# Kernel optimization log

Hardware: AMD Instinct MI355X
Metric: run time of the kernel (lower is better)

The kernel has to match this reference:

```python
import jax, jax.numpy as jnp
import numpy as np

# Problem sizes (see shape_source)
C = 4096                      # sparse matrix is C x C
NUMEL = C * C                 # 16,777,216
S = 3355443                   # round(NUMEL * 0.2) sampled gradient entries
R = 1048576                   # result_quantity (top-k buffer size)
DECAY = 0.95                  # decay_constant
FRAC = S / float(NUMEL)       # fractional_sparsity (mask_active=False branch)


def setup_inputs() -> dict:
    key = jax.random.key(0)
    k1, k2, k3, k4 = jax.random.split(key, 4)
    # Sampled linear indices into the C x C grid (forward: torch.randint(0, numel, [S]))
    sample_index = jax.random.randint(k1, (S,), 0, NUMEL, dtype=jnp.int32)
    # Steady-state buffer of (row, col) pairs and their running gradient magnitudes
    result_index = jax.random.randint(k2, (R, 2), 0, C, dtype=jnp.int32)
    result_value = jax.random.uniform(k3, (R,), dtype=jnp.float32)
    # Incoming gradient on the sampled accumulator entries
    gradient = jax.random.normal(k4, (S,), dtype=jnp.float32)
    return {
        "sample_index": sample_index,
        "result_index": result_index,
        "result_value": result_value,
        "gradient": gradient,
    }


def reference(sample_index, result_index, result_value, gradient):
    """Faithful JAX version of StochasticSubSampler's backward-hook update:
    decay the stored buffer, take |gradient| on the new samples, coalesce
    duplicated (row, col) entries by summation, then keep the top-R values.
    Returns (new_result_index [R,2] int32, new_result_value [R] float32)."""
    adj_decay = 1.0 - FRAC * (1.0 - DECAY)  # adjusted decay constant

    # Linearized keys for coalescing. sample_index is already row*C + col.
    samp_keys = sample_index
    res_keys = result_index[:, 0] * C + result_index[:, 1]
    keys = jnp.concatenate([samp_keys, res_keys])               # [K]
    vals = jnp.concatenate([jnp.abs(gradient), adj_decay * result_value])  # [K]
    K = keys.shape[0]

    # Coalesce: sum values that share the same (row, col) key.
    uniq, inv = jnp.unique(keys, size=K, fill_value=-1, return_inverse=True)
    summed = jax.ops.segment_sum(vals, inv, num_segments=K)     # [K]
    counts = jax.ops.segment_sum(jnp.ones_like(vals), inv, num_segments=K)
    neg = jnp.finfo(jnp.float32).min
    summed = jnp.where(counts > 0, summed, neg)  # mask padded unique slots

    # Descending sort + top-R selection (argsort(-v)[:R] in the original).
    top_vals, top_pos = jax.lax.top_k(summed, R)
    top_keys = uniq[top_pos]
    new_index = jnp.stack([top_keys // C, top_keys % C], axis=-1)  # [R, 2]
    return new_index, top_vals
```

## Files before the change

kernel.cpp:

```cpp
#include <hip/hip_runtime.h>
#include <stdint.h>

#define CDIM   4096
#define S_N    3355443
#define R_N    1048576
#define N1     (S_N + R_N)
#define TILE   4096
#define WPT    (TILE / 256)
#define NTILES ((N1 + TILE - 1) / TILE)
#define NPAD   (NTILES * TILE)
#define NSB    (NPAD / 256)
#define SR_CH  ((NTILES + 255) / 256)
#define PAD_KEY 0xFFFFFFu
#define PAD_VAL 0xFFFFFFFFu
#define SENT  (((uint64_t)PAD_KEY << 32) | (uint64_t)PAD_VAL)

static __device__ __forceinline__ unsigned blockScanExcl(unsigned v, unsigned t,
                                                         unsigned* lw, unsigned* tot){
  unsigned lane = t & 63u, w = t >> 6;
  unsigned x = v;
  #pragma unroll
  for (int off = 1; off < 64; off <<= 1){
    unsigned y = __shfl_up(x, off, 64);
    if (lane >= (unsigned)off) x += y;
  }
  if (lane == 63u) lw[w] = x;
  __syncthreads();
  unsigned woff = 0;
  for (unsigned i = 0; i < w; i++) woff += lw[i];
  *tot = lw[0] + lw[1] + lw[2] + lw[3];
  __syncthreads();
  return x + woff - v;
}

__global__ __launch_bounds__(256) void k_build(const int* __restrict__ sidx,
                                               const int* __restrict__ ridx,
                                               const float* __restrict__ rval,
                                               const float* __restrict__ grad,
                                               uint64_t* __restrict__ A,
                                               unsigned* __restrict__ gh){
  __shared__ unsigned h[256];
  unsigned t = threadIdx.x;
  h[t] = 0; __syncthreads();
  size_t base = (size_t)blockIdx.x * TILE;
  #pragma unroll
  for (int r = 0; r < WPT; r++){
    unsigned i = (unsigned)(base + (size_t)r*256 + t);
    uint32_t key, vb;
    if (i < S_N){
      key = (uint32_t)sidx[i];
      vb  = __float_as_uint(fabsf(grad[i]));
    } else if (i < N1){
      unsigned j = i - S_N;
      int2 rc = ((const int2* __restrict__)ridx)[j];
      key = (uint32_t)(rc.x * CDIM + rc.y);
      const float ADJF = (float)(1.0 - (3355443.0 / 16777216.0) * (1.0 - 0.95));
      vb = __float_as_uint(ADJF * rval[j]);
    } else {
      key = PAD_KEY; vb = PAD_VAL;
    }
    A[i] = ((uint64_t)key << 32) | (uint64_t)vb;
    atomicAdd(&h[key & 0xFFu], 1u);
  }
  __syncthreads();
  gh[t * NTILES + blockIdx.x] = h[t];
}

__global__ __launch_bounds__(256) void k_hist(const uint64_t* __restrict__ in, unsigned shift,
                                              unsigned* __restrict__ gh){
  __shared__ unsigned h[256];
  unsigned t = threadIdx.x;
  h[t] = 0; __syncthreads();
  size_t base = (size_t)blockIdx.x * TILE;
  #pragma unroll
  for (int r = 0; r < WPT; r++){
    uint64_t e = in[base + (size_t)r*256 + t];
    atomicAdd(&h[(unsigned)((e >> shift) & 0xFF)], 1u);
  }
  __syncthreads();
  gh[t * NTILES + blockIdx.x] = h[t];
}

__global__ __launch_bounds__(256) void k_hist_syn(const uint64_t* __restrict__ in, unsigned shift,
                                                  unsigned* __restrict__ gh,
                                                  const unsigned* __restrict__ nsyn){
  __shared__ unsigned h[256];
  unsigned t = threadIdx.x;
  unsigned Un = nsyn[0];
  size_t base = (size_t)blockIdx.x * TILE;
  if (base >= (size_t)Un){
    gh[t * NTILES + blockIdx.x] = (t == 255u) ? (unsigned)TILE : 0u;
    return;
  }
  h[t] = 0; __syncthreads();
  #pragma unroll
  for (int r = 0; r < WPT; r++){
    unsigned i = (unsigned)(base + (size_t)r*256 + t);
    uint64_t e = (i < Un) ? in[i] : SENT;
    atomicAdd(&h[(unsigned)((e >> shift) & 0xFF)], 1u);
  }
  __syncthreads();
  gh[t * NTILES + blockIdx.x] = h[t];
}

__global__ __launch_bounds__(256) void k_scanrows(unsigned* __restrict__ gh,
                                                  unsigned* __restrict__ dtot){
  __shared__ unsigned lw[4];
  unsigned d = blockIdx.x, t = threadIdx.x;
  unsigned rowbase = d * NTILES;
  unsigned vals[SR_CH];
  unsigned s = 0;
  #pragma unroll
  for (int k = 0; k < SR_CH; k++){
    unsigned i = t * SR_CH + (unsigned)k;
    vals[k] = (i < NTILES) ? gh[rowbase + i] : 0u;
    s += vals[k];
  }
  unsigned tot;
  unsigned carry = blockScanExcl(s, t, lw, &tot);
  #pragma unroll
  for (int k = 0; k < SR_CH; k++){
    unsigned i = t * SR_CH + (unsigned)k;
    if (i < NTILES){ gh[rowbase + i] = carry; carry += vals[k]; }
  }
  if (t == 0) dtot[d] = tot;
}

__global__ __launch_bounds__(256) void k_cut(const unsigned* __restrict__ dtot,
                                             unsigned* __restrict__ mvar){
  __shared__ unsigned lw[4];
  unsigned t = threadIdx.x;
  unsigned v = dtot[t];
  unsigned tot;
  unsigned excl = blockScanExcl(v, t, lw, &tot);
  unsigned incl = excl + v;
  if (excl < R_N && incl >= R_N) mvar[0] = incl;
}

template <int MODE>
__device__ __forceinline__ void scatter_body(const uint64_t* __restrict__ in,
                                             uint64_t* __restrict__ out,
                                             float* __restrict__ fout,
                                             unsigned shift,
                                             const unsigned* __restrict__ gh,
                                             const unsigned* __restrict__ dtot,
                                             const unsigned* __restrict__ nsyn,
                                             const unsigned* __restrict__ mskip){
  unsigned Un = 0u, M = 0u;
  if (MODE != 0){
    Un = nsyn[0]; M = mskip[0];
    if ((unsigned)blockIdx.x * TILE >= Un && M <= Un) return;
  }
  __shared__ unsigned wrun[4*256];
  __shared__ unsigned gput[256];
  __shared__ unsigned lw[4];
  __shared__ uint64_t stage[TILE];
  unsigned t = threadIdx.x, lane = t & 63u, w = t >> 6;
  wrun[t] = 0; wrun[256+t] = 0; wrun[512+t] = 0; wrun[768+t] = 0;
  __syncthreads();
  uint64_t ltm = (lane == 0) ? 0ull : (~0ull >> (64u - lane));
  uint64_t elems[WPT]; unsigned rnk[WPT]; unsigned dg[WPT];
  size_t base = (size_t)blockIdx.x * TILE + (size_t)w * (TILE/4);
  #pragma unroll
  for (int r = 0; r < WPT; r++){
    unsigned idx = (unsigned)(base + (size_t)r*64) + lane;
    uint64_t e;
    if (MODE != 0) e = (idx < Un) ? in[idx] : SENT;
    else           e = in[idx];
    elems[r] = e;
    unsigned d = (unsigned)((e >> shift) & 0xFF);
    uint64_t m = ~0ull;
    #pragma unroll
    for (int b = 0; b < 8; b++){
      uint64_t bb = __ballot((d >> b) & 1u);
      m &= ((d >> b) & 1u) ? bb : ~bb;
    }
    unsigned rr   = (unsigned)__popcll(m & ltm);
    unsigned prev = wrun[w*256 + d];
    __builtin_amdgcn_wave_barrier();
    if (rr == 0) wrun[w*256 + d] = prev + (unsigned)__popcll(m);
    __builtin_amdgcn_wave_barrier();
    rnk[r] = prev + rr;
    dg[r]  = d;
  }
  __syncthreads();
  {
    unsigned d = t;
    unsigned c0 = wrun[d], c1 = wrun[256+d], c2 = wrun[512+d], c3 = wrun[768+d];
    unsigned cnt = c0 + c1 + c2 + c3;
    unsigned tot;
    unsigned ldig  = blockScanExcl(cnt, t, lw, &tot);
    unsigned tot2;
    unsigned dbase = blockScanExcl(dtot[d], t, lw, &tot2);
    gput[d] = dbase + gh[d * NTILES + blockIdx.x] - ldig;
    wrun[d]       = ldig;
    wrun[256 + d] = ldig + c0;
    wrun[512 + d] = ldig + c0 + c1;
    wrun[768 + d] = ldig + c0 + c1 + c2;
  }
  __syncthreads();
  #pragma unroll
  for (int r = 0; r < WPT; r++)
    stage[ wrun[w*256 + dg[r]] + rnk[r] ] = elems[r];
  __syncthreads();
  #pragma unroll
  for (int r = 0; r < WPT; r++){
    unsigned j = (unsigned)r * 256u + t;
    uint64_t e = stage[j];
    unsigned d = (unsigned)((e >> shift) & 0xFF);
    unsigned dest = gput[d] + j;
    if (MODE == 2){
      if (dest < R_N){
        uint32_t key = (uint32_t)(e >> 32);
        fout[2u*dest]        = (float)(key >> 12);
        fout[2u*dest + 1u]   = (float)(key & 4095u);
        fout[2u*R_N + dest]  = __uint_as_float(~(uint32_t)e);
      }
    } else if (MODE == 1){
      if (dest < M) out[dest] = e;
    } else {
      out[dest] = e;
    }
  }
}

__global__ __launch_bounds__(256) void k_scatter(const uint64_t* __restrict__ in,
                                                 uint64_t* __restrict__ out,
                                                 unsigned shift,
                                                 const unsigned* __restrict__ gh,
                                                 const unsigned* __restrict__ dtot){
  scatter_body<0>(in, out, nullptr, shift, gh, dtot, nullptr, nullptr);
}

__global__ __launch_bounds__(256) void k_scatter_m(const uint64_t* __restrict__ in,
                                                   uint64_t* __restrict__ out,
                                                   unsigned shift,
                                                   const unsigned* __restrict__ gh,
                                                   const unsigned* __restrict__ dtot,
                                                   const unsigned* __restrict__ nsyn,
                                                   const unsigned* __restrict__ mskip){
  scatter_body<1>(in, out, nullptr, shift, gh, dtot, nsyn, mskip);
}

__global__ __launch_bounds__(256) void k_scatter_out(const uint64_t* __restrict__ in,
                                                     float* __restrict__ fout,
                                                     unsigned shift,
                                                     const unsigned* __restrict__ gh,
                                                     const unsigned* __restrict__ dtot,
                                                     const unsigned* __restrict__ nsyn){
  scatter_body<2>(in, nullptr, fout, shift, gh, dtot, nsyn, nsyn);
}

__global__ __launch_bounds__(256) void k_headcount(const uint64_t* __restrict__ in,
                                                   unsigned* __restrict__ hcnt){
  __shared__ unsigned wc[4];
  unsigned t = threadIdx.x, lane = t & 63u, w = t >> 6;
  size_t p = (size_t)blockIdx.x * 256 + t;
  uint64_t e = in[p];
  uint32_t k = (uint32_t)(e >> 32);
  bool head = ((p == 0) || ((uint32_t)(in[p-1] >> 32) != k)) && ((uint32_t)e != PAD_VAL);
  uint64_t m = __ballot(head);
  if (lane == 0) wc[w] = (unsigned)__popcll(m);
  __syncthreads();
  if (t == 0) hcnt[blockIdx.x] = wc[0] + wc[1] + wc[2] + wc[3];
}

__global__ __launch_bounds__(256) void k_scanheads(unsigned* __restrict__ hcnt,
                                                   unsigned* __restrict__ utot){
  __shared__ unsigned short buf[NSB];
  __shared__ unsigned lw[4];
  unsigned t = threadIdx.x;
  for (unsigned i = t; i < NSB; i += 256) buf[i] = (unsigned short)hcnt[i];
  __syncthreads();
  const unsigned CH = (NSB + 255) / 256;
  unsigned s = 0;
  for (unsigned k = 0; k < CH; k++){
    unsigned i = t * CH + k;
    if (i < NSB) s += buf[i];
  }
  unsigned tot;
  unsigned carry = blockScanExcl(s, t, lw, &tot);
  for (unsigned k = 0; k < CH; k++){
    unsigned i = t * CH + k;
    if (i < NSB){ unsigned v = buf[i]; hcnt[i] = carry; carry += v; }
  }
  if (t == 0) utot[0] = tot;
}

__global__ __launch_bounds__(256) void k_segsum(const uint64_t* __restrict__ in,
                                                uint64_t* __restrict__ out,
                                                const unsigned* __restrict__ hbase){
  __shared__ unsigned wc[4], woffs[4];
  unsigned t = threadIdx.x, lane = t & 63u, w = t >> 6;
  size_t p = (size_t)blockIdx.x * 256 + t;
  uint64_t e0 = in[p];
  uint32_t k = (uint32_t)(e0 >> 32);
  bool head = ((p == 0) || ((uint32_t)(in[p-1] >> 32) != k)) && ((uint32_t)e0 != PAD_VAL);
  uint64_t m = __ballot(head);
  if (lane == 0) wc[w] = (unsigned)__popcll(m);
  __syncthreads();
  if (t == 0){ unsigned a = 0; for (int i = 0; i < 4; i++){ woffs[i] = a; a += wc[i]; } }
  __syncthreads();
  if (head){
    uint64_t ltm = (lane == 0) ? 0ull : (~0ull >> (64u - lane));
    unsigned rank = (unsigned)__popcll(m & ltm);
    unsigned oidx = hbase[blockIdx.x] + woffs[w] + rank;
    float s = __uint_as_float((uint32_t)e0);
    size_t q = p + 1;
    while (q < NPAD){
      uint64_t e = in[q];
      if ((uint32_t)(e >> 32) != k) break;
      uint32_t vb = (uint32_t)e;
      if (vb == PAD_VAL) break;
      s += __uint_as_float(vb);
      q++;
    }
    out[oidx] = ((uint64_t)k << 32) | (uint64_t)(uint32_t)(~__float_as_uint(s));
  }
}

extern "C" void kernel_launch(void* const* d_in, const int* in_sizes, int n_in,
                              void* d_out, int out_size, void* d_ws, size_t ws_size,
                              hipStream_t stream) {
  const int*   sidx = (const int*)d_in[0];
  const int*   ridx = (const int*)d_in[1];
  const float* rval = (const float*)d_in[2];
  const float* grad = (const float*)d_in[3];
  float* out = (float*)d_out;

  uint64_t* A0   = (uint64_t*)d_ws;
  uint64_t* A1   = A0 + NPAD;
  unsigned* gh   = (unsigned*)(A1 + NPAD);
  unsigned* dtot = gh + 256 * NTILES;
  unsigned* hcnt = dtot + 256;
  unsigned* utot = hcnt + NSB;
  unsigned* mvar = utot + 1;

  k_build<<<NTILES, 256, 0, stream>>>(sidx, ridx, rval, grad, A0, gh);

  k_scanrows<<<256,    256, 0, stream>>>(gh, dtot);
  k_scatter <<<NTILES, 256, 0, stream>>>(A0, A1, 32, gh, dtot);
  k_hist    <<<NTILES, 256, 0, stream>>>(A1, 40, gh);
  k_scanrows<<<256,    256, 0, stream>>>(gh, dtot);
  k_scatter <<<NTILES, 256, 0, stream>>>(A1, A0, 40, gh, dtot);
  k_hist    <<<NTILES, 256, 0, stream>>>(A0, 48, gh);
  k_scanrows<<<256,    256, 0, stream>>>(gh, dtot);
  k_scatter <<<NTILES, 256, 0, stream>>>(A0, A1, 48, gh, dtot);

  k_headcount<<<NSB, 256, 0, stream>>>(A1, hcnt);
  k_scanheads<<<1,   256, 0, stream>>>(hcnt, utot);
  k_segsum   <<<NSB, 256, 0, stream>>>(A1, A0, hcnt);

  k_hist_syn <<<NTILES, 256, 0, stream>>>(A0, 24, gh, utot);
  k_scanrows <<<256,    256, 0, stream>>>(gh, dtot);
  k_cut      <<<1,      256, 0, stream>>>(dtot, mvar);
  k_scatter_m<<<NTILES, 256, 0, stream>>>(A0, A1, 24, gh, dtot, utot, mvar);

  k_hist_syn <<<NTILES, 256, 0, stream>>>(A1, 0, gh, mvar);
  k_scanrows <<<256,    256, 0, stream>>>(gh, dtot);
  k_scatter_m<<<NTILES, 256, 0, stream>>>(A1, A0, 0, gh, dtot, mvar, mvar);
  k_hist_syn <<<NTILES, 256, 0, stream>>>(A0, 8, gh, mvar);
  k_scanrows <<<256,    256, 0, stream>>>(gh, dtot);
  k_scatter_m<<<NTILES, 256, 0, stream>>>(A0, A1, 8, gh, dtot, mvar, mvar);
  k_hist_syn <<<NTILES, 256, 0, stream>>>(A1, 16, gh, mvar);
  k_scanrows <<<256,    256, 0, stream>>>(gh, dtot);
  k_scatter_m<<<NTILES, 256, 0, stream>>>(A1, A0, 16, gh, dtot, mvar, mvar);
  k_hist_syn   <<<NTILES, 256, 0, stream>>>(A0, 24, gh, mvar);
  k_scanrows   <<<256,    256, 0, stream>>>(gh, dtot);
  k_scatter_out<<<NTILES, 256, 0, stream>>>(A0, out, 24, gh, dtot, mvar);
}
```

Before: 410.3 us.

## Fuse head-count, scan and segment-sum into single-pass decoupled-lookback coalesce kernel

Replaces the three-kernel coalescing stage (per-block head count, single-block scan, segment sum) with one kernel. It computes per-tile head counts, uses decoupled look-back through a flag/value buffer to get each tile's global output offset, then writes the summed segments. The look-back buffer is zeroed inside the preceding scatter kernel, so no extra memset launch is needed. This saves two launches and one full read of the sorted array, at the cost of inter-block spin-waiting that depends on tiles being scheduled in order.

New measurement: 464.6 us. 1.13x slower.

```diff
diff --git a/kernel.cpp b/kernel.cpp
--- a/kernel.cpp
+++ b/kernel.cpp
@@ -9,7 +9,6 @@
 #define WPT    (TILE / 256)
 #define NTILES ((N1 + TILE - 1) / TILE)
 #define NPAD   (NTILES * TILE)
-#define NSB    (NPAD / 256)
 #define SR_CH  ((NTILES + 255) / 256)
 #define PAD_KEY 0xFFFFFFu
 #define PAD_VAL 0xFFFFFFFFu
@@ -228,7 +227,9 @@
                                                  uint64_t* __restrict__ out,
                                                  unsigned shift,
                                                  const unsigned* __restrict__ gh,
-                                                 const unsigned* __restrict__ dtot){
+                                                 const unsigned* __restrict__ dtot,
+                                                 unsigned* __restrict__ zclr){
+  if (zclr != nullptr && threadIdx.x == 0u) zclr[blockIdx.x] = 0u;
   scatter_body<0>(in, out, nullptr, shift, gh, dtot, nullptr, nullptr);
 }
 
@@ -251,71 +252,101 @@
   scatter_body<2>(in, nullptr, fout, shift, gh, dtot, nsyn, nsyn);
 }
 
-__global__ __launch_bounds__(256) void k_headcount(const uint64_t* __restrict__ in,
-                                                   unsigned* __restrict__ hcnt){
-  __shared__ unsigned wc[4];
-  unsigned t = threadIdx.x, lane = t & 63u, w = t >> 6;
-  size_t p = (size_t)blockIdx.x * 256 + t;
-  uint64_t e = in[p];
-  uint32_t k = (uint32_t)(e >> 32);
-  bool head = ((p == 0) || ((uint32_t)(in[p-1] >> 32) != k)) && ((uint32_t)e != PAD_VAL);
-  uint64_t m = __ballot(head);
-  if (lane == 0) wc[w] = (unsigned)__popcll(m);
-  __syncthreads();
-  if (t == 0) hcnt[blockIdx.x] = wc[0] + wc[1] + wc[2] + wc[3];
-}
-
-__global__ __launch_bounds__(256) void k_scanheads(unsigned* __restrict__ hcnt,
-                                                   unsigned* __restrict__ utot){
-  __shared__ unsigned short buf[NSB];
-  __shared__ unsigned lw[4];
-  unsigned t = threadIdx.x;
-  for (unsigned i = t; i < NSB; i += 256) buf[i] = (unsigned short)hcnt[i];
-  __syncthreads();
-  const unsigned CH = (NSB + 255) / 256;
-  unsigned s = 0;
-  for (unsigned k = 0; k < CH; k++){
-    unsigned i = t * CH + k;
-    if (i < NSB) s += buf[i];
-  }
-  unsigned tot;
-  unsigned carry = blockScanExcl(s, t, lw, &tot);
-  for (unsigned k = 0; k < CH; k++){
-    unsigned i = t * CH + k;
-    if (i < NSB){ unsigned v = buf[i]; hcnt[i] = carry; carry += v; }
-  }
-  if (t == 0) utot[0] = tot;
-}
-
-__global__ __launch_bounds__(256) void k_segsum(const uint64_t* __restrict__ in,
-                                                uint64_t* __restrict__ out,
-                                                const unsigned* __restrict__ hbase){
-  __shared__ unsigned wc[4], woffs[4];
-  unsigned t = threadIdx.x, lane = t & 63u, w = t >> 6;
-  size_t p = (size_t)blockIdx.x * 256 + t;
-  uint64_t e0 = in[p];
-  uint32_t k = (uint32_t)(e0 >> 32);
-  bool head = ((p == 0) || ((uint32_t)(in[p-1] >> 32) != k)) && ((uint32_t)e0 != PAD_VAL);
-  uint64_t m = __ballot(head);
-  if (lane == 0) wc[w] = (unsigned)__popcll(m);
-  __syncthreads();
-  if (t == 0){ unsigned a = 0; for (int i = 0; i < 4; i++){ woffs[i] = a; a += wc[i]; } }
-  __syncthreads();
-  if (head){
-    uint64_t ltm = (lane == 0) ? 0ull : (~0ull >> (64u - lane));
-    unsigned rank = (unsigned)__popcll(m & ltm);
-    unsigned oidx = hbase[blockIdx.x] + woffs[w] + rank;
-    float s = __uint_as_float((uint32_t)e0);
-    size_t q = p + 1;
-    while (q < NPAD){
-      uint64_t e = in[q];
-      if ((uint32_t)(e >> 32) != k) break;
-      uint32_t vb = (uint32_t)e;
-      if (vb == PAD_VAL) break;
-      s += __uint_as_float(vb);
-      q++;
-    }
-    out[oidx] = ((uint64_t)k << 32) | (uint64_t)(uint32_t)(~__float_as_uint(s));
+__global__ __launch_bounds__(256) void k_coalesce(const uint64_t* __restrict__ in,
+                                                  uint64_t* __restrict__ out,
+                                                  unsigned* __restrict__ lb,
+                                                  unsigned* __restrict__ utot){
+  __shared__ unsigned wrc[64];
+  __shared__ unsigned woffs[64];
+  __shared__ unsigned hb;
+  unsigned b = blockIdx.x, t = threadIdx.x, lane = t & 63u, w = t >> 6;
+  size_t base = (size_t)b * TILE;
+  unsigned flags = 0u;
+  #pragma unroll
+  for (int r = 0; r < WPT; r++){
+    size_t p = base + (size_t)r*256 + t;
+    uint64_t e = in[p];
+    uint32_t k = (uint32_t)(e >> 32);
+    uint32_t kp = (uint32_t)__shfl_up((int)k, 1, 64);
+    if (lane == 0u) kp = (p == 0) ? 0u : (uint32_t)(in[p-1] >> 32);
+    bool head = ((p == 0) || (kp != k)) && ((uint32_t)e != PAD_VAL);
+    flags |= (head ? 1u : 0u) << r;
+    unsigned long long m = __ballot(head);
+    if (lane == 0u) wrc[(unsigned)r*4u + w] = (unsigned)__popcll(m);
+  }
+  __syncthreads();
+  if (w == 0u){
+    unsigned v = wrc[lane];
+    unsigned x = v;
+    #pragma unroll
+    for (int off = 1; off < 64; off <<= 1){
+      unsigned y = __shfl_up(x, off, 64);
+      if (lane >= (unsigned)off) x += y;
+    }
+    woffs[lane] = x - v;
+    unsigned cnt = (unsigned)__shfl((int)x, 63);
+    if (lane == 0u)
+      __hip_atomic_store(&lb[b], ((b == 0u) ? (2u<<30) : (1u<<30)) | cnt,
+                         __ATOMIC_RELEASE, __HIP_MEMORY_SCOPE_AGENT);
+    unsigned run = 0u;
+    if (b > 0u){
+      int p0 = (int)b - 1;
+      for (;;){
+        int idx = p0 - (int)lane;
+        unsigned v2 = (idx >= 0)
+          ? __hip_atomic_load(&lb[idx], __ATOMIC_ACQUIRE, __HIP_MEMORY_SCOPE_AGENT)
+          : (2u << 30);
+        if (__ballot((v2 >> 30) == 0u)){ __builtin_amdgcn_s_sleep(1); continue; }
+        unsigned long long im = __ballot((v2 >> 30) == 2u);
+        unsigned cv = v2 & 0x3FFFFFFFu;
+        unsigned contrib;
+        bool fin = (im != 0ull);
+        if (fin){
+          unsigned li = (unsigned)__ffsll((long long)im) - 1u;
+          contrib = (lane <= li) ? cv : 0u;
+        } else {
+          contrib = cv;
+        }
+        #pragma unroll
+        for (int off = 1; off < 64; off <<= 1)
+          contrib += (unsigned)__shfl_xor((int)contrib, off, 64);
+        run += contrib;
+        if (fin) break;
+        p0 -= 64;
+      }
+      if (lane == 0u)
+        __hip_atomic_store(&lb[b], (2u<<30) | (run + cnt),
+                           __ATOMIC_RELEASE, __HIP_MEMORY_SCOPE_AGENT);
+    }
+    if (lane == 0u){
+      hb = run;
+      if (b == (unsigned)(NTILES - 1)) utot[0] = run + cnt;
+    }
+  }
+  __syncthreads();
+  unsigned hbase = hb;
+  #pragma unroll
+  for (int r = 0; r < WPT; r++){
+    bool f = ((flags >> r) & 1u) != 0u;
+    unsigned long long m = __ballot(f);
+    if (f){
+      size_t p = base + (size_t)r*256 + t;
+      uint64_t e0 = in[p];
+      uint32_t k = (uint32_t)(e0 >> 32);
+      unsigned long long ltm = (lane == 0u) ? 0ull : (~0ull >> (64u - lane));
+      unsigned rank = woffs[(unsigned)r*4u + w] + (unsigned)__popcll(m & ltm);
+      float s = __uint_as_float((uint32_t)e0);
+      size_t q = p + 1;
+      while (q < NPAD){
+        uint64_t e = in[q];
+        if ((uint32_t)(e >> 32) != k) break;
+        uint32_t vb = (uint32_t)e;
+        if (vb == PAD_VAL) break;
+        s += __uint_as_float(vb);
+        q++;
+      }
+      out[hbase + rank] = ((uint64_t)k << 32) | (uint64_t)(uint32_t)(~__float_as_uint(s));
+    }
   }
 }
 
@@ -332,24 +363,22 @@
   uint64_t* A1   = A0 + NPAD;
   unsigned* gh   = (unsigned*)(A1 + NPAD);
   unsigned* dtot = gh + 256 * NTILES;
-  unsigned* hcnt = dtot + 256;
-  unsigned* utot = hcnt + NSB;
+  unsigned* lbuf = dtot + 256;
+  unsigned* utot = lbuf + NTILES;
   unsigned* mvar = utot + 1;
 
   k_build<<<NTILES, 256, 0, stream>>>(sidx, ridx, rval, grad, A0, gh);
 
   k_scanrows<<<256,    256, 0, stream>>>(gh, dtot);
-  k_scatter <<<NTILES, 256, 0, stream>>>(A0, A1, 32, gh, dtot);
+  k_scatter <<<NTILES, 256, 0, stream>>>(A0, A1, 32, gh, dtot, nullptr);
   k_hist    <<<NTILES, 256, 0, stream>>>(A1, 40, gh);
   k_scanrows<<<256,    256, 0, stream>>>(gh, dtot);
-  k_scatter <<<NTILES, 256, 0, stream>>>(A1, A0, 40, gh, dtot);
+  k_scatter <<<NTILES, 256, 0, stream>>>(A1, A0, 40, gh, dtot, nullptr);
   k_hist    <<<NTILES, 256, 0, stream>>>(A0, 48, gh);
   k_scanrows<<<256,    256, 0, stream>>>(gh, dtot);
-  k_scatter <<<NTILES, 256, 0, stream>>>(A0, A1, 48, gh, dtot);
-
-  k_headcount<<<NSB, 256, 0, stream>>>(A1, hcnt);
-  k_scanheads<<<1,   256, 0, stream>>>(hcnt, utot);
-  k_segsum   <<<NSB, 256, 0, stream>>>(A1, A0, hcnt);
+  k_scatter <<<NTILES, 256, 0, stream>>>(A0, A1, 48, gh, dtot, lbuf);
+
+  k_coalesce<<<NTILES, 256, 0, stream>>>(A1, A0, lbuf, utot);
 
   k_hist_syn <<<NTILES, 256, 0, stream>>>(A0, 24, gh, utot);
   k_scanrows <<<256,    256, 0, stream>>>(gh, dtot);
```

## Fuse element build into first radix scatter and fold cut into scatter

Applied to the files above, without the earlier changes.

The build kernel no longer materializes the packed 64-bit key/value array. A histogram-only pass reads just the low key byte, and the first scatter pass builds the elements on the fly from the raw inputs. This removes one full write and one read of the roughly 35 MB intermediate array. The separate single-block cut kernel is also removed: each block of the first top-k scatter computes the cutoff itself from the digit totals, and block 0 publishes it. The cost is a more complex scatter template and some redundant per-block cut computation.

After: 412.1 us. Within noise of the previous version (+0.4%).

```diff
diff --git a/kernel.cpp b/kernel.cpp
--- a/kernel.cpp
+++ b/kernel.cpp
@@ -14,6 +14,7 @@
 #define PAD_KEY 0xFFFFFFu
 #define PAD_VAL 0xFFFFFFFFu
 #define SENT  (((uint64_t)PAD_KEY << 32) | (uint64_t)PAD_VAL)
+#define ADJF  ((float)(1.0 - (3355443.0 / 16777216.0) * (1.0 - 0.95)))
 
 static __device__ __forceinline__ unsigned blockScanExcl(unsigned v, unsigned t,
                                                          unsigned* lw, unsigned* tot){
@@ -33,11 +34,28 @@
   return x + woff - v;
 }
 
-__global__ __launch_bounds__(256) void k_build(const int* __restrict__ sidx,
+static __device__ __forceinline__ uint64_t make_elem(unsigned i,
+                                                     const int* __restrict__ sidx,
+                                                     const int* __restrict__ ridx,
+                                                     const float* __restrict__ rval,
+                                                     const float* __restrict__ grad){
+  uint32_t key, vb;
+  if (i < S_N){
+    key = (uint32_t)sidx[i];
+    vb  = __float_as_uint(fabsf(grad[i]));
+  } else if (i < N1){
+    unsigned j = i - S_N;
+    int2 rc = ((const int2* __restrict__)ridx)[j];
+    key = (uint32_t)(rc.x * CDIM + rc.y);
+    vb = __float_as_uint(ADJF * rval[j]);
+  } else {
+    key = PAD_KEY; vb = PAD_VAL;
+  }
+  return ((uint64_t)key << 32) | (uint64_t)vb;
+}
+
+__global__ __launch_bounds__(256) void k_hist0(const int* __restrict__ sidx,
                                                const int* __restrict__ ridx,
-                                               const float* __restrict__ rval,
-                                               const float* __restrict__ grad,
-                                               uint64_t* __restrict__ A,
                                                unsigned* __restrict__ gh){
   __shared__ unsigned h[256];
   unsigned t = threadIdx.x;
@@ -46,21 +64,11 @@
   #pragma unroll
   for (int r = 0; r < WPT; r++){
     unsigned i = (unsigned)(base + (size_t)r*256 + t);
-    uint32_t key, vb;
-    if (i < S_N){
-      key = (uint32_t)sidx[i];
-      vb  = __float_as_uint(fabsf(grad[i]));
-    } else if (i < N1){
-      unsigned j = i - S_N;
-      int2 rc = ((const int2* __restrict__)ridx)[j];
-      key = (uint32_t)(rc.x * CDIM + rc.y);
-      const float ADJF = (float)(1.0 - (3355443.0 / 16777216.0) * (1.0 - 0.95));
-      vb = __float_as_uint(ADJF * rval[j]);
-    } else {
-      key = PAD_KEY; vb = PAD_VAL;
-    }
-    A[i] = ((uint64_t)key << 32) | (uint64_t)vb;
-    atomicAdd(&h[key & 0xFFu], 1u);
+    unsigned kb;
+    if (i < S_N)       kb = ((uint32_t)sidx[i]) & 0xFFu;
+    else if (i < N1)   kb = ((uint32_t)ridx[2u*(i - S_N) + 1u]) & 0xFFu;
+    else               kb = 0xFFu;
+    atomicAdd(&h[kb], 1u);
   }
   __syncthreads();
   gh[t * NTILES + blockIdx.x] = h[t];
@@ -126,17 +134,6 @@
   if (t == 0) dtot[d] = tot;
 }
 
-__global__ __launch_bounds__(256) void k_cut(const unsigned* __restrict__ dtot,
-                                             unsigned* __restrict__ mvar){
-  __shared__ unsigned lw[4];
-  unsigned t = threadIdx.x;
-  unsigned v = dtot[t];
-  unsigned tot;
-  unsigned excl = blockScanExcl(v, t, lw, &tot);
-  unsigned incl = excl + v;
-  if (excl < R_N && incl >= R_N) mvar[0] = incl;
-}
-
 template <int MODE>
 __device__ __forceinline__ void scatter_body(const uint64_t* __restrict__ in,
                                              uint64_t* __restrict__ out,
@@ -145,15 +142,24 @@
                                              const unsigned* __restrict__ gh,
                                              const unsigned* __restrict__ dtot,
                                              const unsigned* __restrict__ nsyn,
-                                             const unsigned* __restrict__ mskip){
+                                             const unsigned* __restrict__ mskip,
+                                             const int* __restrict__ sidx,
+                                             const int* __restrict__ ridx,
+                                             const float* __restrict__ rval,
+                                             const float* __restrict__ grad,
+                                             unsigned* __restrict__ mout){
   unsigned Un = 0u, M = 0u;
-  if (MODE != 0){
-    Un = nsyn[0]; M = mskip[0];
-    if ((unsigned)blockIdx.x * TILE >= Un && M <= Un) return;
+  if (MODE == 1 || MODE == 2 || MODE == 4){
+    Un = nsyn[0];
+    if (MODE != 4){
+      M = mskip[0];
+      if ((unsigned)blockIdx.x * TILE >= Un && M <= Un) return;
+    }
   }
   __shared__ unsigned wrun[4*256];
   __shared__ unsigned gput[256];
   __shared__ unsigned lw[4];
+  __shared__ unsigned cutm;
   __shared__ uint64_t stage[TILE];
   unsigned t = threadIdx.x, lane = t & 63u, w = t >> 6;
   wrun[t] = 0; wrun[256+t] = 0; wrun[512+t] = 0; wrun[768+t] = 0;
@@ -165,8 +171,9 @@
   for (int r = 0; r < WPT; r++){
     unsigned idx = (unsigned)(base + (size_t)r*64) + lane;
     uint64_t e;
-    if (MODE != 0) e = (idx < Un) ? in[idx] : SENT;
-    else           e = in[idx];
+    if (MODE == 3)      e = make_elem(idx, sidx, ridx, rval, grad);
+    else if (MODE != 0) e = (idx < Un) ? in[idx] : SENT;
+    else                e = in[idx];
     elems[r] = e;
     unsigned d = (unsigned)((e >> shift) & 0xFF);
     uint64_t m = ~0ull;
@@ -192,6 +199,10 @@
     unsigned ldig  = blockScanExcl(cnt, t, lw, &tot);
     unsigned tot2;
     unsigned dbase = blockScanExcl(dtot[d], t, lw, &tot2);
+    if (MODE == 4){
+      unsigned incl = dbase + dtot[d];
+      if (dbase < R_N && incl >= R_N) cutm = incl;
+    }
     gput[d] = dbase + gh[d * NTILES + blockIdx.x] - ldig;
     wrun[d]       = ldig;
     wrun[256 + d] = ldig + c0;
@@ -199,6 +210,10 @@
     wrun[768 + d] = ldig + c0 + c1 + c2;
   }
   __syncthreads();
+  if (MODE == 4){
+    M = cutm;
+    if (blockIdx.x == 0u && t == 0u) mout[0] = M;
+  }
   #pragma unroll
   for (int r = 0; r < WPT; r++)
     stage[ wrun[w*256 + dg[r]] + rnk[r] ] = elems[r];
@@ -216,7 +231,7 @@
         fout[2u*dest + 1u]   = (float)(key & 4095u);
         fout[2u*R_N + dest]  = __uint_as_float(~(uint32_t)e);
       }
-    } else if (MODE == 1){
+    } else if (MODE == 1 || MODE == 4){
       if (dest < M) out[dest] = e;
     } else {
       out[dest] = e;
@@ -229,7 +244,20 @@
                                                  unsigned shift,
                                                  const unsigned* __restrict__ gh,
                                                  const unsigned* __restrict__ dtot){
-  scatter_body<0>(in, out, nullptr, shift, gh, dtot, nullptr, nullptr);
+  scatter_body<0>(in, out, nullptr, shift, gh, dtot, nullptr, nullptr,
+                  nullptr, nullptr, nullptr, nullptr, nullptr);
+}
+
+__global__ __launch_bounds__(256) void k_scatter_b(const int* __restrict__ sidx,
+                                                   const int* __restrict__ ridx,
+                                                   const float* __restrict__ rval,
+                                                   const float* __restrict__ grad,
+                                                   uint64_t* __restrict__ out,
+                                                   unsigned shift,
+                                                   const unsigned* __restrict__ gh,
+                                                   const unsigned* __restrict__ dtot){
+  scatter_body<3>(nullptr, out, nullptr, shift, gh, dtot, nullptr, nullptr,
+                  sidx, ridx, rval, grad, nullptr);
 }
 
 __global__ __launch_bounds__(256) void k_scatter_m(const uint64_t* __restrict__ in,
@@ -239,7 +267,19 @@
                                                    const unsigned* __restrict__ dtot,
                                                    const unsigned* __restrict__ nsyn,
                                                    const unsigned* __restrict__ mskip){
-  scatter_body<1>(in, out, nullptr, shift, gh, dtot, nsyn, mskip);
+  scatter_body<1>(in, out, nullptr, shift, gh, dtot, nsyn, mskip,
+                  nullptr, nullptr, nullptr, nullptr, nullptr);
+}
+
+__global__ __launch_bounds__(256) void k_scatter_mc(const uint64_t* __restrict__ in,
+                                                    uint64_t* __restrict__ out,
+                                                    unsigned shift,
+                                                    const unsigned* __restrict__ gh,
+                                                    const unsigned* __restrict__ dtot,
+                                                    const unsigned* __restrict__ nsyn,
+                                                    unsigned* __restrict__ mout){
+  scatter_body<4>(in, out, nullptr, shift, gh, dtot, nsyn, nullptr,
+                  nullptr, nullptr, nullptr, nullptr, mout);
 }
 
 __global__ __launch_bounds__(256) void k_scatter_out(const uint64_t* __restrict__ in,
@@ -248,7 +288,8 @@
                                                      const unsigned* __restrict__ gh,
                                                      const unsigned* __restrict__ dtot,
                                                      const unsigned* __restrict__ nsyn){
-  scatter_body<2>(in, nullptr, fout, shift, gh, dtot, nsyn, nsyn);
+  scatter_body<2>(in, nullptr, fout, shift, gh, dtot, nsyn, nsyn,
+                  nullptr, nullptr, nullptr, nullptr, nullptr);
 }
 
 __global__ __launch_bounds__(256) void k_headcount(const uint64_t* __restrict__ in,
@@ -336,25 +377,23 @@
   unsigned* utot = hcnt + NSB;
   unsigned* mvar = utot + 1;
 
-  k_build<<<NTILES, 256, 0, stream>>>(sidx, ridx, rval, grad, A0, gh);
-
-  k_scanrows<<<256,    256, 0, stream>>>(gh, dtot);
-  k_scatter <<<NTILES, 256, 0, stream>>>(A0, A1, 32, gh, dtot);
-  k_hist    <<<NTILES, 256, 0, stream>>>(A1, 40, gh);
-  k_scanrows<<<256,    256, 0, stream>>>(gh, dtot);
-  k_scatter <<<NTILES, 256, 0, stream>>>(A1, A0, 40, gh, dtot);
-  k_hist    <<<NTILES, 256, 0, stream>>>(A0, 48, gh);
-  k_scanrows<<<256,    256, 0, stream>>>(gh, dtot);
-  k_scatter <<<NTILES, 256, 0, stream>>>(A0, A1, 48, gh, dtot);
+  k_hist0    <<<NTILES, 256, 0, stream>>>(sidx, ridx, gh);
+  k_scanrows <<<256,    256, 0, stream>>>(gh, dtot);
+  k_scatter_b<<<NTILES, 256, 0, stream>>>(sidx, ridx, rval, grad, A1, 32, gh, dtot);
+  k_hist     <<<NTILES, 256, 0, stream>>>(A1, 40, gh);
+  k_scanrows <<<256,    256, 0, stream>>>(gh, dtot);
+  k_scatter  <<<NTILES, 256, 0, stream>>>(A1, A0, 40, gh, dtot);
+  k_hist     <<<NTILES, 256, 0, stream>>>(A0, 48, gh);
+  k_scanrows <<<256,    256, 0, stream>>>(gh, dtot);
+  k_scatter  <<<NTILES, 256, 0, stream>>>(A0, A1, 48, gh, dtot);
 
   k_headcount<<<NSB, 256, 0, stream>>>(A1, hcnt);
   k_scanheads<<<1,   256, 0, stream>>>(hcnt, utot);
   k_segsum   <<<NSB, 256, 0, stream>>>(A1, A0, hcnt);
 
-  k_hist_syn <<<NTILES, 256, 0, stream>>>(A0, 24, gh, utot);
-  k_scanrows <<<256,    256, 0, stream>>>(gh, dtot);
-  k_cut      <<<1,      256, 0, stream>>>(dtot, mvar);
-  k_scatter_m<<<NTILES, 256, 0, stream>>>(A0, A1, 24, gh, dtot, utot, mvar);
+  k_hist_syn  <<<NTILES, 256, 0, stream>>>(A0, 24, gh, utot);
+  k_scanrows  <<<256,    256, 0, stream>>>(gh, dtot);
+  k_scatter_mc<<<NTILES, 256, 0, stream>>>(A0, A1, 24, gh, dtot, utot, mvar);
 
   k_hist_syn <<<NTILES, 256, 0, stream>>>(A1, 0, gh, mvar);
   k_scanrows <<<256,    256, 0, stream>>>(gh, dtot);
```
